# Kernel tuning notes

Hardware: AMD Instinct MI355X
Metric: run time of the kernel (lower is better)

Reference implementation:

```python
import jax, jax.numpy as jnp
import numpy as np

N_HEADS = 8
KEY_DIM = 64
MEM_DIM = 64
HEAD_DIM = 64
IN_DIM = 256
OUT_DIM = 256


def setup_inputs() -> dict:
    key = jax.random.key(0)
    ks = jax.random.split(key, 7)
    x = jax.random.normal(ks[0], (8, IN_DIM, 64, 64), dtype=jnp.float32)
    # learned params
    key_p = jax.random.uniform(ks[1], (N_HEADS, KEY_DIM, MEM_DIM), dtype=jnp.float32)
    memory = jax.random.uniform(ks[2], (N_HEADS, MEM_DIM, HEAD_DIM), dtype=jnp.float32) * 0.5 - 0.25
    w_in = jax.random.normal(ks[3], (N_HEADS * KEY_DIM, IN_DIM), dtype=jnp.float32) * (1.0 / np.sqrt(IN_DIM))
    b_in = jax.random.normal(ks[4], (N_HEADS * KEY_DIM,), dtype=jnp.float32) * 0.01
    w_out = jax.random.normal(ks[5], (OUT_DIM, N_HEADS * HEAD_DIM), dtype=jnp.float32) * (1.0 / np.sqrt(N_HEADS * HEAD_DIM))
    b_out = jax.random.normal(ks[6], (OUT_DIM,), dtype=jnp.float32) * 0.01
    return {"x": x, "key_p": key_p, "memory": memory, "w_in": w_in, "b_in": b_in, "w_out": w_out, "b_out": b_out}


def reference(x, key_p, memory, w_in, b_in, w_out, b_out):
    B, _, H, W = x.shape
    # 1x1 conv projection: [B, n_heads*key_dim, H, W]
    out = jnp.einsum('oc,bchw->bohw', w_in, x) + b_in[None, :, None, None]
    # split heads: b (k n) h w -> b n k h w  (einops '(c m)' with m=n_heads => c is outer)
    out = out.reshape(B, KEY_DIM, N_HEADS, H, W).transpose(0, 2, 1, 3, 4)
    # per-head key matmul over key_dim -> memory_dim
    out = jnp.einsum('nkm,bnkhw->bnmhw', key_p, out)
    out = jax.nn.softmax(out, axis=2)
    # per-head memory matmul over memory_dim -> head_dim
    out = jnp.einsum('nmd,bnmhw->bndhw', memory, out)
    # merge heads: b n d h w -> b (d n) h w  (einops 'b m c h w -> b (m c) h w' with m=heads... wait)
    # einops 'b m c h w -> b (m c) h w': m (heads) is outer -> transpose then reshape
    out = out.reshape(B, N_HEADS * HEAD_DIM, H, W)
    # final 1x1 conv
    out = jnp.einsum('oc,bchw->bohw', w_out, out) + b_out[None, :, None, None]
    return out
```

## Files before the change

kernel.cpp:

```cpp
#include <hip/hip_runtime.h>


typedef _Float16 half8 __attribute__((ext_vector_type(8)));
typedef _Float16 half4 __attribute__((ext_vector_type(4)));
typedef _Float16 half2v __attribute__((ext_vector_type(2)));
typedef float float4v __attribute__((ext_vector_type(4)));

__global__ __launch_bounds__(256) void fold_all(
    const float* __restrict__ key_p, const float* __restrict__ w_in,
    const float* __restrict__ b_in, const float* __restrict__ w_out,
    const float* __restrict__ memory,
    _Float16* __restrict__ Aswz, _Float16* __restrict__ Mswz, float* __restrict__ bb)
{
    __shared__ float sv[512];
    __shared__ float red[64];
    const int blk = blockIdx.x;
    const int t = threadIdx.x;

    if (blk < 512) {
        const int row = blk, n = row >> 6, m = row & 63;
        if (t < 64) sv[t] = key_p[n * 4096 + t * 64 + m];
        __syncthreads();
        const int c = t;
        float v = 0.f;
        #pragma unroll 16
        for (int k = 0; k < 64; ++k)
            v = fmaf(sv[k], w_in[(k * 8 + n) * 256 + c], v);
        int R = row >> 4, s = c >> 5, i = c & 7;
        int l = (row & 15) + 16 * ((c >> 3) & 3);
        Aswz[(((R * 8 + s) * 64 + l) << 3) + i] = (_Float16)v;
        if (t < 64) red[t] = sv[t] * b_in[t * 8 + n];
        __syncthreads();
        if (t == 0) {
            float s2 = 0.f;
            for (int k = 0; k < 64; ++k) s2 += red[k];
            bb[row] = s2;
        }
    } else {
        const int o = blk - 512;
        sv[t]       = w_out[o * 512 + t];
        sv[256 + t] = w_out[o * 512 + 256 + t];
        __syncthreads();
        #pragma unroll
        for (int hh = 0; hh < 2; ++hh) {
            int col = t + hh * 256, n = col >> 6, m = col & 63;
            const float4* mrow = (const float4*)(memory + n * 4096 + m * 64);
            const float4* wrow = (const float4*)(sv + n * 64);
            float v = 0.f;
            #pragma unroll
            for (int qd = 0; qd < 16; ++qd) {
                float4 a = mrow[qd], w = wrow[qd];
                v += a.x * w.x + a.y * w.y + a.z * w.z + a.w * w.w;
            }
            int R2 = o >> 4, s = col >> 5, i = col & 7;
            int l = (o & 15) + 16 * ((col >> 3) & 3);
            Mswz[(((R2 * 16 + s) * 64 + l) << 3) + i] = (_Float16)v;
        }
    }
}

#define XS_STRIDE 264

__global__ __launch_bounds__(256, 2) void fused_main(
    const float* __restrict__ x, const _Float16* __restrict__ Aswz,
    const float* __restrict__ bb, const _Float16* __restrict__ Mswz,
    const float* __restrict__ b_out, float* __restrict__ out)
{
    __shared__ _Float16 S[32768];

    const int t  = threadIdx.x;
    const int w  = t >> 6;
    const int l  = t & 63;
    const int q  = l >> 4;
    const int lp = l & 15;
    const int wg  = blockIdx.x;
    const int b   = wg >> 6;
    const int hw0 = (wg & 63) * 64;
    const float* xb = x + (size_t)b * 256 * 4096 + hw0;

    #pragma unroll
    for (int i = 0; i < 8; ++i) {
        int u  = i * 256 + t;
        int cp = u & 127;
        int qq = u >> 7;
        int c0 = cp * 2, p4 = qq * 4;
        const float* px = xb + (size_t)c0 * 4096 + p4;
        float4 v0 = *(const float4*)(px);
        float4 v1 = *(const float4*)(px + 4096);
        *(half2v*)(&S[(p4 + 0) * XS_STRIDE + c0]) = half2v{(_Float16)v0.x, (_Float16)v1.x};
        *(half2v*)(&S[(p4 + 1) * XS_STRIDE + c0]) = half2v{(_Float16)v0.y, (_Float16)v1.y};
        *(half2v*)(&S[(p4 + 2) * XS_STRIDE + c0]) = half2v{(_Float16)v0.z, (_Float16)v1.z};
        *(half2v*)(&S[(p4 + 3) * XS_STRIDE + c0]) = half2v{(_Float16)v0.w, (_Float16)v1.w};
    }
    __syncthreads();

    float4v acc[8][4];
    #pragma unroll
    for (int r = 0; r < 8; ++r)
        #pragma unroll
        for (int c = 0; c < 4; ++c) acc[r][c] = float4v{0.f, 0.f, 0.f, 0.f};

    const half8* Ag = (const half8*)Aswz;
    for (int s = 0; s < 8; ++s) {
        half8 bf[4];
        #pragma unroll
        for (int c = 0; c < 4; ++c)
            bf[c] = *(const half8*)(&S[(c * 16 + lp) * XS_STRIDE + s * 32 + q * 8]);
        half8 af[8];
        #pragma unroll
        for (int r = 0; r < 8; ++r)
            af[r] = Ag[((w * 8 + r) * 8 + s) * 64 + l];
        #pragma unroll
        for (int r = 0; r < 8; ++r)
            #pragma unroll
            for (int c = 0; c < 4; ++c)
                acc[r][c] = __builtin_amdgcn_mfma_f32_16x16x32_f16(af[r], bf[c], acc[r][c], 0, 0, 0);
    }

    #pragma unroll
    for (int r = 0; r < 8; ++r) {
        float4v bbv = *(const float4v*)(bb + w * 128 + r * 16 + q * 4);
        #pragma unroll
        for (int c = 0; c < 4; ++c)
            #pragma unroll
            for (int j = 0; j < 4; ++j) acc[r][c][j] += bbv[j];
    }

    __syncthreads();

    #pragma unroll
    for (int h = 0; h < 2; ++h) {
        #pragma unroll
        for (int c = 0; c < 4; ++c) {
            float mx = -1e30f;
            #pragma unroll
            for (int rr = 0; rr < 4; ++rr) {
                int r = h * 4 + rr;
                #pragma unroll
                for (int j = 0; j < 4; ++j) mx = fmaxf(mx, acc[r][c][j]);
            }
            mx = fmaxf(mx, __shfl_xor(mx, 16, 64));
            mx = fmaxf(mx, __shfl_xor(mx, 32, 64));
            float sum = 0.f;
            #pragma unroll
            for (int rr = 0; rr < 4; ++rr) {
                int r = h * 4 + rr;
                #pragma unroll
                for (int j = 0; j < 4; ++j) {
                    float e = __expf(acc[r][c][j] - mx);
                    acc[r][c][j] = e;
                    sum += e;
                }
            }
            sum += __shfl_xor(sum, 16, 64);
            sum += __shfl_xor(sum, 32, 64);
            float inv = 1.f / sum;
            #pragma unroll
            for (int rr = 0; rr < 4; ++rr) {
                int r = h * 4 + rr;
                int s2 = w * 4 + (r >> 1);
                int lq = ((r & 1) * 2 + (q >> 1)) * 16 + lp;
                int i0 = (q & 1) * 4;
                half4 pv = {(_Float16)(acc[r][c][0] * inv), (_Float16)(acc[r][c][1] * inv),
                            (_Float16)(acc[r][c][2] * inv), (_Float16)(acc[r][c][3] * inv)};
                *(half4*)(&S[(((s2 * 4 + c) * 64) + lq) * 8 + i0]) = pv;
            }
        }
    }
    __syncthreads();

    float4v acc2[4][4];
    #pragma unroll
    for (int r = 0; r < 4; ++r)
        #pragma unroll
        for (int c = 0; c < 4; ++c) acc2[r][c] = float4v{0.f, 0.f, 0.f, 0.f};

    const half8* Mg = (const half8*)Mswz;
    for (int s2 = 0; s2 < 16; ++s2) {
        half8 bf2[4];
        #pragma unroll
        for (int c = 0; c < 4; ++c)
            bf2[c] = *(const half8*)(&S[(((s2 * 4 + c) * 64) + l) * 8]);
        half8 af2[4];
        #pragma unroll
        for (int r = 0; r < 4; ++r)
            af2[r] = Mg[((w * 4 + r) * 16 + s2) * 64 + l];
        #pragma unroll
        for (int r = 0; r < 4; ++r)
            #pragma unroll
            for (int c = 0; c < 4; ++c)
                acc2[r][c] = __builtin_amdgcn_mfma_f32_16x16x32_f16(af2[r], bf2[c], acc2[r][c], 0, 0, 0);
    }

    float* Sf = (float*)S;
    #pragma unroll
    for (int pass = 0; pass < 2; ++pass) {
        __syncthreads();
        if ((w >> 1) == pass) {
            int rbase = (w & 1) * 64;
            #pragma unroll
            for (int r = 0; r < 4; ++r)
                #pragma unroll
                for (int j = 0; j < 4; ++j)
                    #pragma unroll
                    for (int c = 0; c < 4; ++c)
                        Sf[(rbase + r * 16 + q * 4 + j) * 68 + c * 16 + lp] = acc2[r][c][j];
        }
        __syncthreads();
        #pragma unroll
        for (int it = 0; it < 8; ++it) {
            int flat = it * 256 + t;
            int row  = flat >> 4;
            int ch   = flat & 15;
            float4 v = *(const float4*)(&Sf[row * 68 + ch * 4]);
            int o = pass * 128 + row;
            float bo = b_out[o];
            v.x += bo; v.y += bo; v.z += bo; v.w += bo;
            *(float4*)(out + ((size_t)b * 256 + o) * 4096 + hw0 + ch * 4) = v;
        }
    }
}

extern "C" void kernel_launch(void* const* d_in, const int* in_sizes, int n_in,
                              void* d_out, int out_size, void* d_ws, size_t ws_size,
                              hipStream_t stream) {
    (void)in_sizes; (void)n_in; (void)ws_size; (void)out_size;
    const float* x      = (const float*)d_in[0];
    const float* key_p  = (const float*)d_in[1];
    const float* memory = (const float*)d_in[2];
    const float* w_in   = (const float*)d_in[3];
    const float* b_in   = (const float*)d_in[4];
    const float* w_out  = (const float*)d_in[5];
    const float* b_out  = (const float*)d_in[6];
    float* out = (float*)d_out;

    _Float16* Aswz = (_Float16*)d_ws;
    _Float16* Mswz = Aswz + 512 * 256;
    float*    bb   = (float*)(Mswz + 256 * 512);

    fold_all<<<768, 256, 0, stream>>>(key_p, w_in, b_in, w_out, memory, Aswz, Mswz, bb);
    fused_main<<<512, 256, 0, stream>>>(x, Aswz, bb, Mswz, b_out, out);
}
```

Before: 120.2 us.

## Halve LDS footprint by staging softmax output in two halves, raise occupancy

The softmax probabilities are now written to shared memory in two halves. The first half of the heads is stored and consumed by the second GEMM while the other half is held in registers, then written and consumed in a second pass. The memory-weight swizzle is re-indexed so the K-steps line up with this split. Shared memory drops from 64KB to about 34KB and launch bounds are raised to 4 blocks per CU to improve latency hiding. The cost is an extra barrier pair, more live registers, and a register cap under the higher occupancy that could cause spills.

```diff
diff --git a/kernel.cpp b/kernel.cpp
--- a/kernel.cpp
+++ b/kernel.cpp
@@ -52,21 +52,23 @@
                 float4 a = mrow[qd], w = wrow[qd];
                 v += a.x * w.x + a.y * w.y + a.z * w.z + a.w * w.w;
             }
-            int R2 = o >> 4, s = col >> 5, i = col & 7;
-            int l = (o & 15) + 16 * ((col >> 3) & 3);
+            int R2 = o >> 4, i = col & 7;
+            int s = ((n & 1) << 3) + ((n >> 1) << 1) + (m >> 5);
+            int l = (o & 15) + 16 * ((m >> 3) & 3);
             Mswz[(((R2 * 16 + s) * 64 + l) << 3) + i] = (_Float16)v;
         }
     }
 }
 
 #define XS_STRIDE 264
-
-__global__ __launch_bounds__(256, 2) void fused_main(
+#define SF_STRIDE 68
+
+__global__ __launch_bounds__(256, 4) void fused_main(
     const float* __restrict__ x, const _Float16* __restrict__ Aswz,
     const float* __restrict__ bb, const _Float16* __restrict__ Mswz,
     const float* __restrict__ b_out, float* __restrict__ out)
 {
-    __shared__ _Float16 S[32768];
+    __shared__ _Float16 S[17408];
 
     const int t  = threadIdx.x;
     const int w  = t >> 6;
@@ -128,6 +130,7 @@
 
     __syncthreads();
 
+    half4 ph[4][4];
     #pragma unroll
     for (int h = 0; h < 2; ++h) {
         #pragma unroll
@@ -158,12 +161,16 @@
             #pragma unroll
             for (int rr = 0; rr < 4; ++rr) {
                 int r = h * 4 + rr;
-                int s2 = w * 4 + (r >> 1);
-                int lq = ((r & 1) * 2 + (q >> 1)) * 16 + lp;
-                int i0 = (q & 1) * 4;
                 half4 pv = {(_Float16)(acc[r][c][0] * inv), (_Float16)(acc[r][c][1] * inv),
                             (_Float16)(acc[r][c][2] * inv), (_Float16)(acc[r][c][3] * inv)};
-                *(half4*)(&S[(((s2 * 4 + c) * 64) + lq) * 8 + i0]) = pv;
+                if (h == 0) {
+                    int s2c = w * 2 + (rr >> 1);
+                    int lq = ((rr & 1) * 2 + (q >> 1)) * 16 + lp;
+                    int i0 = (q & 1) * 4;
+                    *(half4*)(&S[(((s2c * 4 + c) * 64) + lq) * 8 + i0]) = pv;
+                } else {
+                    ph[rr][c] = pv;
+                }
             }
         }
     }
@@ -176,15 +183,43 @@
         for (int c = 0; c < 4; ++c) acc2[r][c] = float4v{0.f, 0.f, 0.f, 0.f};
 
     const half8* Mg = (const half8*)Mswz;
-    for (int s2 = 0; s2 < 16; ++s2) {
+    for (int sc = 0; sc < 8; ++sc) {
         half8 bf2[4];
         #pragma unroll
         for (int c = 0; c < 4; ++c)
-            bf2[c] = *(const half8*)(&S[(((s2 * 4 + c) * 64) + l) * 8]);
+            bf2[c] = *(const half8*)(&S[(((sc * 4 + c) * 64) + l) * 8]);
         half8 af2[4];
         #pragma unroll
         for (int r = 0; r < 4; ++r)
-            af2[r] = Mg[((w * 4 + r) * 16 + s2) * 64 + l];
+            af2[r] = Mg[((w * 4 + r) * 16 + sc) * 64 + l];
+        #pragma unroll
+        for (int r = 0; r < 4; ++r)
+            #pragma unroll
+            for (int c = 0; c < 4; ++c)
+                acc2[r][c] = __builtin_amdgcn_mfma_f32_16x16x32_f16(af2[r], bf2[c], acc2[r][c], 0, 0, 0);
+    }
+    __syncthreads();
+
+    #pragma unroll
+    for (int rr = 0; rr < 4; ++rr) {
+        int s2c = w * 2 + (rr >> 1);
+        int lq = ((rr & 1) * 2 + (q >> 1)) * 16 + lp;
+        int i0 = (q & 1) * 4;
+        #pragma unroll
+        for (int c = 0; c < 4; ++c)
+            *(half4*)(&S[(((s2c * 4 + c) * 64) + lq) * 8 + i0]) = ph[rr][c];
+    }
+    __syncthreads();
+
+    for (int sc = 0; sc < 8; ++sc) {
+        half8 bf2[4];
+        #pragma unroll
+        for (int c = 0; c < 4; ++c)
+            bf2[c] = *(const half8*)(&S[(((sc * 4 + c) * 64) + l) * 8]);
+        half8 af2[4];
+        #pragma unroll
+        for (int r = 0; r < 4; ++r)
+            af2[r] = Mg[((w * 4 + r) * 16 + 8 + sc) * 64 + l];
         #pragma unroll
         for (int r = 0; r < 4; ++r)
             #pragma unroll
@@ -204,7 +239,7 @@
                 for (int j = 0; j < 4; ++j)
                     #pragma unroll
                     for (int c = 0; c < 4; ++c)
-                        Sf[(rbase + r * 16 + q * 4 + j) * 68 + c * 16 + lp] = acc2[r][c][j];
+                        Sf[(rbase + r * 16 + q * 4 + j) * SF_STRIDE + c * 16 + lp] = acc2[r][c][j];
         }
         __syncthreads();
         #pragma unroll
@@ -212,7 +247,7 @@
             int flat = it * 256 + t;
             int row  = flat >> 4;
             int ch   = flat & 15;
-            float4 v = *(const float4*)(&Sf[row * 68 + ch * 4]);
+            float4 v = *(const float4*)(&Sf[row * SF_STRIDE + ch * 4]);
             int o = pass * 128 + row;
             float bo = b_out[o];
             v.x += bo; v.y += bo; v.z += bo; v.w += bo;
```

After: 213.8 us. +77.8%, slower.

## Halve pixel tile per block to double grid and raise occupancy

Applied to the files above, without the earlier changes.

The main fused kernel now handles 32 pixels per workgroup instead of 64, launching 1024 blocks with launch bounds of 4 waves-per-SIMD occupancy. Shared memory and accumulator registers shrink accordingly, and the output staging is done in one pass with a narrower stride. The fold kernel's bias reduction uses wavefront shuffles instead of a shared array and extra barrier. The smaller tile means each A/M weight fragment loaded from global memory feeds fewer MFMAs, so weight traffic per pixel doubles.

```diff
diff --git a/kernel.cpp b/kernel.cpp
--- a/kernel.cpp
+++ b/kernel.cpp
@@ -13,7 +13,6 @@
     _Float16* __restrict__ Aswz, _Float16* __restrict__ Mswz, float* __restrict__ bb)
 {
     __shared__ float sv[512];
-    __shared__ float red[64];
     const int blk = blockIdx.x;
     const int t = threadIdx.x;
 
@@ -29,12 +28,15 @@
         int R = row >> 4, s = c >> 5, i = c & 7;
         int l = (row & 15) + 16 * ((c >> 3) & 3);
         Aswz[(((R * 8 + s) * 64 + l) << 3) + i] = (_Float16)v;
-        if (t < 64) red[t] = sv[t] * b_in[t * 8 + n];
-        __syncthreads();
-        if (t == 0) {
-            float s2 = 0.f;
-            for (int k = 0; k < 64; ++k) s2 += red[k];
-            bb[row] = s2;
+        if (t < 64) {
+            float rv = sv[t] * b_in[t * 8 + n];
+            rv += __shfl_xor(rv, 32, 64);
+            rv += __shfl_xor(rv, 16, 64);
+            rv += __shfl_xor(rv, 8, 64);
+            rv += __shfl_xor(rv, 4, 64);
+            rv += __shfl_xor(rv, 2, 64);
+            rv += __shfl_xor(rv, 1, 64);
+            if (t == 0) bb[row] = rv;
         }
     } else {
         const int o = blk - 512;
@@ -60,13 +62,14 @@
 }
 
 #define XS_STRIDE 264
-
-__global__ __launch_bounds__(256, 2) void fused_main(
+#define SF_STRIDE 36
+
+__global__ __launch_bounds__(256, 4) void fused_main(
     const float* __restrict__ x, const _Float16* __restrict__ Aswz,
     const float* __restrict__ bb, const _Float16* __restrict__ Mswz,
     const float* __restrict__ b_out, float* __restrict__ out)
 {
-    __shared__ _Float16 S[32768];
+    __shared__ _Float16 S[18432];
 
     const int t  = threadIdx.x;
     const int w  = t >> 6;
@@ -74,12 +77,12 @@
     const int q  = l >> 4;
     const int lp = l & 15;
     const int wg  = blockIdx.x;
-    const int b   = wg >> 6;
-    const int hw0 = (wg & 63) * 64;
+    const int b   = wg >> 7;
+    const int hw0 = (wg & 127) * 32;
     const float* xb = x + (size_t)b * 256 * 4096 + hw0;
 
     #pragma unroll
-    for (int i = 0; i < 8; ++i) {
+    for (int i = 0; i < 4; ++i) {
         int u  = i * 256 + t;
         int cp = u & 127;
         int qq = u >> 7;
@@ -94,34 +97,38 @@
     }
     __syncthreads();
 
-    float4v acc[8][4];
+    float4v acc[8][2];
     #pragma unroll
     for (int r = 0; r < 8; ++r)
         #pragma unroll
-        for (int c = 0; c < 4; ++c) acc[r][c] = float4v{0.f, 0.f, 0.f, 0.f};
+        for (int c = 0; c < 2; ++c) acc[r][c] = float4v{0.f, 0.f, 0.f, 0.f};
 
     const half8* Ag = (const half8*)Aswz;
     for (int s = 0; s < 8; ++s) {
-        half8 bf[4];
-        #pragma unroll
-        for (int c = 0; c < 4; ++c)
+        half8 bf[2];
+        #pragma unroll
+        for (int c = 0; c < 2; ++c)
             bf[c] = *(const half8*)(&S[(c * 16 + lp) * XS_STRIDE + s * 32 + q * 8]);
-        half8 af[8];
-        #pragma unroll
-        for (int r = 0; r < 8; ++r)
-            af[r] = Ag[((w * 8 + r) * 8 + s) * 64 + l];
-        #pragma unroll
-        for (int r = 0; r < 8; ++r)
-            #pragma unroll
-            for (int c = 0; c < 4; ++c)
-                acc[r][c] = __builtin_amdgcn_mfma_f32_16x16x32_f16(af[r], bf[c], acc[r][c], 0, 0, 0);
+        #pragma unroll
+        for (int rh = 0; rh < 2; ++rh) {
+            half8 af4[4];
+            #pragma unroll
+            for (int rr = 0; rr < 4; ++rr)
+                af4[rr] = Ag[((w * 8 + rh * 4 + rr) * 8 + s) * 64 + l];
+            #pragma unroll
+            for (int rr = 0; rr < 4; ++rr)
+                #pragma unroll
+                for (int c = 0; c < 2; ++c)
+                    acc[rh * 4 + rr][c] =
+                        __builtin_amdgcn_mfma_f32_16x16x32_f16(af4[rr], bf[c], acc[rh * 4 + rr][c], 0, 0, 0);
+        }
     }
 
     #pragma unroll
     for (int r = 0; r < 8; ++r) {
         float4v bbv = *(const float4v*)(bb + w * 128 + r * 16 + q * 4);
         #pragma unroll
-        for (int c = 0; c < 4; ++c)
+        for (int c = 0; c < 2; ++c)
             #pragma unroll
             for (int j = 0; j < 4; ++j) acc[r][c][j] += bbv[j];
     }
@@ -131,7 +138,7 @@
     #pragma unroll
     for (int h = 0; h < 2; ++h) {
         #pragma unroll
-        for (int c = 0; c < 4; ++c) {
+        for (int c = 0; c < 2; ++c) {
             float mx = -1e30f;
             #pragma unroll
             for (int rr = 0; rr < 4; ++rr) {
@@ -158,66 +165,59 @@
             #pragma unroll
             for (int rr = 0; rr < 4; ++rr) {
                 int r = h * 4 + rr;
-                int s2 = w * 4 + (r >> 1);
-                int lq = ((r & 1) * 2 + (q >> 1)) * 16 + lp;
-                int i0 = (q & 1) * 4;
+                int sc  = w * 4 + h * 2 + (rr >> 1);
+                int sub = (rr & 1) * 2 + (q >> 1);
+                int i0  = (q & 1) * 4;
                 half4 pv = {(_Float16)(acc[r][c][0] * inv), (_Float16)(acc[r][c][1] * inv),
                             (_Float16)(acc[r][c][2] * inv), (_Float16)(acc[r][c][3] * inv)};
-                *(half4*)(&S[(((s2 * 4 + c) * 64) + lq) * 8 + i0]) = pv;
-            }
-        }
-    }
-    __syncthreads();
-
-    float4v acc2[4][4];
+                *(half4*)(&S[(((sc * 2 + c) * 64) + sub * 16 + lp) * 8 + i0]) = pv;
+            }
+        }
+    }
+    __syncthreads();
+
+    float4v acc2[4][2];
     #pragma unroll
     for (int r = 0; r < 4; ++r)
         #pragma unroll
-        for (int c = 0; c < 4; ++c) acc2[r][c] = float4v{0.f, 0.f, 0.f, 0.f};
+        for (int c = 0; c < 2; ++c) acc2[r][c] = float4v{0.f, 0.f, 0.f, 0.f};
 
     const half8* Mg = (const half8*)Mswz;
-    for (int s2 = 0; s2 < 16; ++s2) {
-        half8 bf2[4];
-        #pragma unroll
-        for (int c = 0; c < 4; ++c)
-            bf2[c] = *(const half8*)(&S[(((s2 * 4 + c) * 64) + l) * 8]);
+    for (int sc = 0; sc < 16; ++sc) {
+        half8 bf2[2];
+        #pragma unroll
+        for (int c = 0; c < 2; ++c)
+            bf2[c] = *(const half8*)(&S[(((sc * 2 + c) * 64) + l) * 8]);
         half8 af2[4];
         #pragma unroll
         for (int r = 0; r < 4; ++r)
-            af2[r] = Mg[((w * 4 + r) * 16 + s2) * 64 + l];
+            af2[r] = Mg[((w * 4 + r) * 16 + sc) * 64 + l];
         #pragma unroll
         for (int r = 0; r < 4; ++r)
             #pragma unroll
-            for (int c = 0; c < 4; ++c)
+            for (int c = 0; c < 2; ++c)
                 acc2[r][c] = __builtin_amdgcn_mfma_f32_16x16x32_f16(af2[r], bf2[c], acc2[r][c], 0, 0, 0);
     }
+    __syncthreads();
 
     float* Sf = (float*)S;
     #pragma unroll
-    for (int pass = 0; pass < 2; ++pass) {
-        __syncthreads();
-        if ((w >> 1) == pass) {
-            int rbase = (w & 1) * 64;
-            #pragma unroll
-            for (int r = 0; r < 4; ++r)
-                #pragma unroll
-                for (int j = 0; j < 4; ++j)
-                    #pragma unroll
-                    for (int c = 0; c < 4; ++c)
-                        Sf[(rbase + r * 16 + q * 4 + j) * 68 + c * 16 + lp] = acc2[r][c][j];
-        }
-        __syncthreads();
-        #pragma unroll
-        for (int it = 0; it < 8; ++it) {
-            int flat = it * 256 + t;
-            int row  = flat >> 4;
-            int ch   = flat & 15;
-            float4 v = *(const float4*)(&Sf[row * 68 + ch * 4]);
-            int o = pass * 128 + row;
-            float bo = b_out[o];
-            v.x += bo; v.y += bo; v.z += bo; v.w += bo;
-            *(float4*)(out + ((size_t)b * 256 + o) * 4096 + hw0 + ch * 4) = v;
-        }
+    for (int r = 0; r < 4; ++r)
+        #pragma unroll
+        for (int j = 0; j < 4; ++j)
+            #pragma unroll
+            for (int c = 0; c < 2; ++c)
+                Sf[(w * 64 + r * 16 + q * 4 + j) * SF_STRIDE + c * 16 + lp] = acc2[r][c][j];
+    __syncthreads();
+    #pragma unroll
+    for (int it = 0; it < 8; ++it) {
+        int flat = it * 256 + t;
+        int row  = flat >> 3;
+        int ch   = flat & 7;
+        float4 v = *(const float4*)(&Sf[row * SF_STRIDE + ch * 4]);
+        float bo = b_out[row];
+        v.x += bo; v.y += bo; v.z += bo; v.w += bo;
+        *(float4*)(out + ((size_t)b * 256 + row) * 4096 + hw0 + ch * 4) = v;
     }
 }
 
@@ -239,5 +239,5 @@
     float*    bb   = (float*)(Mswz + 256 * 512);
 
     fold_all<<<768, 256, 0, stream>>>(key_p, w_in, b_in, w_out, memory, Aswz, Mswz, bb);
-    fused_main<<<512, 256, 0, stream>>>(x, Aswz, bb, Mswz, b_out, out);
+    fused_main<<<1024, 256, 0, stream>>>(x, Aswz, bb, Mswz, b_out, out);
 }
```

Result: slower. 126.5 us (+5.2%).
